# Kernel tuning notes

Measured on AMD Instinct MI355X. Metric: run time of the kernel, lower is better.

Reference implementation:

```python
import jax, jax.numpy as jnp
import numpy as np

NUM_HEADS = 12


def setup_inputs() -> dict:
    key = jax.random.key(0)
    ks = jax.random.split(key, 6)
    dim = 384
    B, N = 2048, 49
    nW = 64
    return {
        "x": jax.random.normal(ks[0], (B, N, dim), dtype=jnp.float32),
        "mask": jax.random.normal(ks[1], (nW, N, N), dtype=jnp.float32),
        "qkv_w": jax.random.normal(ks[2], (3 * dim, dim), dtype=jnp.float32) * 0.02,
        "qkv_b": jax.random.normal(ks[3], (3 * dim,), dtype=jnp.float32) * 0.02,
        "proj_w": jax.random.normal(ks[4], (dim, dim), dtype=jnp.float32) * 0.02,
        "proj_b": jax.random.normal(ks[5], (dim,), dtype=jnp.float32) * 0.02,
    }


def reference(x, mask, qkv_w, qkv_b, proj_w, proj_b):
    B, N, C = x.shape
    H = NUM_HEADS
    Dh = C // H
    scale = Dh ** -0.5
    nW = mask.shape[0]

    # qkv projection: [B, N, 3C]
    qkv = x @ qkv_w.T + qkv_b
    q, k, v = jnp.split(qkv, 3, axis=-1)

    def heads(t):  # [B, N, C] -> [B, H, N, Dh]
        return t.reshape(B, N, H, Dh).transpose(0, 2, 1, 3)

    q, k, v = heads(q) * scale, heads(k), heads(v)

    # [B, H, N, N] attention scores
    attn = jnp.einsum("bhnd,bhmd->bhnm", q, k)
    # add per-window additive mask: reshape B -> (B//nW, nW)
    attn = attn.reshape(B // nW, nW, H, N, N) + mask[None, :, None, :, :]
    attn = jax.nn.softmax(attn.reshape(B, H, N, N), axis=-1)

    out = jnp.einsum("bhnm,bhmd->bhnd", attn, v)
    out = out.transpose(0, 2, 1, 3).reshape(B, N, C)
    return out @ proj_w.T + proj_b
```

## Files before the change

### kernel.cpp

```cpp
#include <hip/hip_runtime.h>
#include <hip/hip_bf16.h>
#include <stdint.h>

typedef unsigned short u16;
typedef __attribute__((ext_vector_type(8))) short short8;
typedef __attribute__((ext_vector_type(4))) short s4v;
typedef __attribute__((ext_vector_type(4))) float f32x4;

__device__ inline u16 f2bf(float f) {
    union { float f; unsigned int u; } x; x.f = f;
    unsigned int u = x.u;
    unsigned int r = (u + 0x7FFFu + ((u >> 16) & 1u)) >> 16;
    return (u16)r;
}

__device__ inline void gld_lds16(const u16* g, u16* l) {
    auto const* gp = reinterpret_cast<const __attribute__((address_space(1))) unsigned int*>(
        reinterpret_cast<uintptr_t>(g));
    auto* lp = reinterpret_cast<__attribute__((address_space(3))) unsigned int*>(
        reinterpret_cast<uintptr_t>(l));
    __builtin_amdgcn_global_load_lds(gp, lp, 16, 0, 0);
}

#if __has_builtin(__builtin_amdgcn_mfma_f32_16x16x16bf16_1k)
#define MFMA16(a, b, c) __builtin_amdgcn_mfma_f32_16x16x16bf16_1k((a), (b), (c), 0, 0, 0)
#elif __has_builtin(__builtin_amdgcn_mfma_f32_16x16x16_bf16)
#define MFMA16(a, b, c) __builtin_amdgcn_mfma_f32_16x16x16_bf16((a), (b), (c), 0, 0, 0)
#else
__device__ inline f32x4 mfma16_asm(s4v a, s4v b, f32x4 c) {
    asm volatile("s_nop 1\n\tv_mfma_f32_16x16x16_bf16 %0, %1, %2, %0\n\ts_nop 7\n\ts_nop 7"
                 : "+v"(c) : "v"(a), "v"(b));
    return c;
}
#define MFMA16(a, b, c) mfma16_asm((a), (b), (c))
#endif

#define NX8 4816896
#define NQ8 55296
#define NP8 18432
__global__ __launch_bounds__(256) void prep_all(const float* __restrict__ x,
                                                const float* __restrict__ qw,
                                                const float* __restrict__ pw,
                                                u16* __restrict__ xb,
                                                u16* __restrict__ wq,
                                                u16* __restrict__ wp) {
    size_t i = (size_t)blockIdx.x * 256 + threadIdx.x;
    const float* src; u16* dst; size_t off;
    if (i < NX8)            { src = x;  dst = xb; off = i; }
    else if (i < NX8 + NQ8) { src = qw; dst = wq; off = i - NX8; }
    else                    { src = pw; dst = wp; off = i - (NX8 + NQ8); }
    float4 v0 = ((const float4*)src)[off * 2];
    float4 v1 = ((const float4*)src)[off * 2 + 1];
    u16 h[8];
    h[0] = f2bf(v0.x); h[1] = f2bf(v0.y); h[2] = f2bf(v0.z); h[3] = f2bf(v0.w);
    h[4] = f2bf(v1.x); h[5] = f2bf(v1.y); h[6] = f2bf(v1.z); h[7] = f2bf(v1.w);
    *(uint4*)(dst + off * 8) = *(const uint4*)h;
}

__global__ __launch_bounds__(256) void qkv_gemm(const u16* __restrict__ xb,
                                                const u16* __restrict__ wq,
                                                const float* __restrict__ bias,
                                                u16* __restrict__ qkv_out) {
    __shared__ u16 As[128 * 32];
    __shared__ u16 Bs[128 * 32];
    const int tid = threadIdx.x;
    const int wave = tid >> 6, lane = tid & 63;
    const int lr = lane >> 4, lc = lane & 15;
    const int wm = (wave & 1) * 64, wn = (wave >> 1) * 64;
    const int lin = blockIdx.x;
    const int xcd = lin & 7;
    const int idx = lin >> 3;
    const int nBase = (idx % 9) * 128;
    const int mBase = (xcd * 98 + idx / 9) * 128;

    f32x4 acc[4][4] = {};

    const int srow = lane >> 2, scol = (lane & 3) * 8;
    const u16* aSrc = xb + (size_t)(mBase + wave * 32 + srow) * 384 + scol;
    const u16* bSrc = wq + (size_t)(nBase + wave * 32 + srow) * 384 + scol;
    u16* aDst = &As[wave * 1024];
    u16* bDst = &Bs[wave * 1024];

    for (int k0 = 0; k0 < 384; k0 += 32) {
        gld_lds16(aSrc + k0, aDst);
        gld_lds16(aSrc + k0 + (size_t)16 * 384, aDst + 512);
        gld_lds16(bSrc + k0, bDst);
        gld_lds16(bSrc + k0 + (size_t)16 * 384, bDst + 512);
        __syncthreads();
        short8 af[4], bfr[4];
#pragma unroll
        for (int i = 0; i < 4; ++i)
            af[i] = *(const short8*)&As[(wm + i * 16 + lc) * 32 + lr * 8];
#pragma unroll
        for (int j = 0; j < 4; ++j)
            bfr[j] = *(const short8*)&Bs[(wn + j * 16 + lc) * 32 + lr * 8];
#pragma unroll
        for (int i = 0; i < 4; ++i)
#pragma unroll
            for (int j = 0; j < 4; ++j)
                acc[i][j] = __builtin_amdgcn_mfma_f32_16x16x32_bf16(bfr[j], af[i], acc[i][j], 0, 0, 0);
        __syncthreads();
    }

    const float scale = 0.17677669529663687f;
#pragma unroll
    for (int j = 0; j < 4; ++j) {
        int gnb = nBase + wn + j * 16 + lr * 4;
        float4 bv = *(const float4*)&bias[gnb];
        float mult = (gnb < 384) ? scale : 1.0f;
#pragma unroll
        for (int i = 0; i < 4; ++i) {
            int gm = mBase + wm + i * 16 + lc;
            union { u16 h[4]; uint2 u; } pk;
            pk.h[0] = f2bf((acc[i][j][0] + bv.x) * mult);
            pk.h[1] = f2bf((acc[i][j][1] + bv.y) * mult);
            pk.h[2] = f2bf((acc[i][j][2] + bv.z) * mult);
            pk.h[3] = f2bf((acc[i][j][3] + bv.w) * mult);
            *(uint2*)(qkv_out + (size_t)gm * 1152 + gnb) = pk.u;
        }
    }
}

__global__ __launch_bounds__(256, 3) void attn_kernel(const u16* __restrict__ qkv,
                                                      const float* __restrict__ mask,
                                                      u16* __restrict__ aout) {
#define PST 68
    __shared__ u16 Vt_s[4][32 * PST];
    const int tid = threadIdx.x;
    const int wave = tid >> 6, lane = tid & 63;
    const int lr = lane >> 4, lc = lane & 15;
    const int bid = blockIdx.x;
    const int b = bid / 3;
    const int h = (bid - b * 3) * 4 + wave;
    const int w = b & 63;
    const float* mrow = mask + (size_t)w * 2401;

    const u16* Q = qkv + (size_t)b * 49 * 1152 + h * 32;
    const u16* K = Q + 384;
    const u16* V = Q + 768;

    {
        u16 vv[32];
        if (lane < 49) {
#pragma unroll
            for (int c = 0; c < 4; ++c)
                *(uint4*)&vv[c * 8] = *(const uint4*)(V + (size_t)lane * 1152 + c * 8);
        } else {
#pragma unroll
            for (int c = 0; c < 32; ++c) vv[c] = 0;
        }
#pragma unroll
        for (int d = 0; d < 32; ++d)
            Vt_s[wave][d * PST + lane] = vv[d];
    }

    short8 qf[4], kf[4];
    const short8 z8 = {0, 0, 0, 0, 0, 0, 0, 0};
#pragma unroll
    for (int i = 0; i < 4; ++i) {
        int row = i * 16 + lc;
        qf[i] = (row < 49) ? *(const short8*)(Q + (size_t)row * 1152 + lr * 8) : z8;
        kf[i] = (row < 49) ? *(const short8*)(K + (size_t)row * 1152 + lr * 8) : z8;
    }

    __syncthreads();

    s4v vfA[2][4];
#pragma unroll
    for (int nt = 0; nt < 2; ++nt)
#pragma unroll
        for (int sj = 0; sj < 4; ++sj)
            vfA[nt][sj] = *(const s4v*)&Vt_s[wave][(nt * 16 + lc) * PST + sj * 16 + lr * 4];

    f32x4 S2[4][4] = {};
#pragma unroll
    for (int si = 0; si < 4; ++si)
#pragma unroll
        for (int sj = 0; sj < 4; ++sj)
            S2[si][sj] = __builtin_amdgcn_mfma_f32_16x16x32_bf16(kf[sj], qf[si], S2[si][sj], 0, 0, 0);

    const size_t orow = (size_t)b * 49 * 384 + h * 32 + lr * 4;
#pragma unroll
    for (int si = 0; si < 4; ++si) {
        int q = si * 16 + lc;
        int im = (q < 49) ? q : 48;
        const float* mq = mrow + im * 49;
        float s = 0.0f;
        s4v pfq[4];
#pragma unroll
        for (int sj = 0; sj < 4; ++sj) {
            int kbase = sj * 16 + lr * 4;
            s4v pk;
#pragma unroll
            for (int r = 0; r < 4; ++r) {
                int k = kbase + r;
                float t = (k < 49) ? (S2[si][sj][r] + mq[k]) : -1e30f;
                float p = __expf(t);
                s += p;
                pk[r] = (short)f2bf(p);
            }
            pfq[sj] = pk;
        }
        s += __shfl_xor(s, 16);
        s += __shfl_xor(s, 32);

        f32x4 O0 = {}, O1 = {};
#pragma unroll
        for (int sj = 0; sj < 4; ++sj) {
            O0 = MFMA16(vfA[0][sj], pfq[sj], O0);
            O1 = MFMA16(vfA[1][sj], pfq[sj], O1);
        }

        if (q < 49) {
            float rl = __builtin_amdgcn_rcpf(s);
            union { u16 h[4]; uint2 u; } pk;
            pk.h[0] = f2bf(O0[0] * rl); pk.h[1] = f2bf(O0[1] * rl);
            pk.h[2] = f2bf(O0[2] * rl); pk.h[3] = f2bf(O0[3] * rl);
            *(uint2*)(aout + orow + (size_t)q * 384) = pk.u;
            pk.h[0] = f2bf(O1[0] * rl); pk.h[1] = f2bf(O1[1] * rl);
            pk.h[2] = f2bf(O1[2] * rl); pk.h[3] = f2bf(O1[3] * rl);
            *(uint2*)(aout + orow + (size_t)q * 384 + 16) = pk.u;
        }
    }
#undef PST
}

__global__ __launch_bounds__(256) void proj_gemm(const u16* __restrict__ a,
                                                 const u16* __restrict__ wp,
                                                 const float* __restrict__ bias,
                                                 float* __restrict__ out) {
    __shared__ u16 As[128 * 32];
    __shared__ u16 Bs[128 * 32];
    const int tid = threadIdx.x;
    const int wave = tid >> 6, lane = tid & 63;
    const int lr = lane >> 4, lc = lane & 15;
    const int wm = (wave & 1) * 64, wn = (wave >> 1) * 64;
    const int lin = blockIdx.x;
    const int xcd = lin & 7;
    const int idx = lin >> 3;
    const int nBase = (idx % 3) * 128;
    const int mBase = (xcd * 98 + idx / 3) * 128;

    f32x4 acc[4][4] = {};

    const int srow = lane >> 2, scol = (lane & 3) * 8;
    const u16* aSrc = a  + (size_t)(mBase + wave * 32 + srow) * 384 + scol;
    const u16* bSrc = wp + (size_t)(nBase + wave * 32 + srow) * 384 + scol;
    u16* aDst = &As[wave * 1024];
    u16* bDst = &Bs[wave * 1024];

    for (int k0 = 0; k0 < 384; k0 += 32) {
        gld_lds16(aSrc + k0, aDst);
        gld_lds16(aSrc + k0 + (size_t)16 * 384, aDst + 512);
        gld_lds16(bSrc + k0, bDst);
        gld_lds16(bSrc + k0 + (size_t)16 * 384, bDst + 512);
        __syncthreads();
        short8 af[4], bfr[4];
#pragma unroll
        for (int i = 0; i < 4; ++i)
            af[i] = *(const short8*)&As[(wm + i * 16 + lc) * 32 + lr * 8];
#pragma unroll
        for (int j = 0; j < 4; ++j)
            bfr[j] = *(const short8*)&Bs[(wn + j * 16 + lc) * 32 + lr * 8];
#pragma unroll
        for (int i = 0; i < 4; ++i)
#pragma unroll
            for (int j = 0; j < 4; ++j)
                acc[i][j] = __builtin_amdgcn_mfma_f32_16x16x32_bf16(bfr[j], af[i], acc[i][j], 0, 0, 0);
        __syncthreads();
    }

#pragma unroll
    for (int j = 0; j < 4; ++j) {
        int gnb = nBase + wn + j * 16 + lr * 4;
        float4 bv = *(const float4*)&bias[gnb];
#pragma unroll
        for (int i = 0; i < 4; ++i) {
            int gm = mBase + wm + i * 16 + lc;
            float4 o;
            o.x = acc[i][j][0] + bv.x;
            o.y = acc[i][j][1] + bv.y;
            o.z = acc[i][j][2] + bv.z;
            o.w = acc[i][j][3] + bv.w;
            *(float4*)(out + (size_t)gm * 384 + gnb) = o;
        }
    }
}

extern "C" void kernel_launch(void* const* d_in, const int* in_sizes, int n_in,
                              void* d_out, int out_size, void* d_ws, size_t ws_size,
                              hipStream_t stream) {
    const float* x      = (const float*)d_in[0];
    const float* mask   = (const float*)d_in[1];
    const float* qkv_w  = (const float*)d_in[2];
    const float* qkv_b  = (const float*)d_in[3];
    const float* proj_w = (const float*)d_in[4];
    const float* proj_b = (const float*)d_in[5];
    float* out = (float*)d_out;

    char* ws = (char*)d_ws;
    u16* wq   = (u16*)ws;
    u16* wp   = (u16*)(ws + 884736);
    u16* qkvb = (u16*)(ws + 1179648);
    u16* xb   = (u16*)(ws + 232390656);
    u16* attn = xb;

    prep_all<<<19104, 256, 0, stream>>>(x, qkv_w, proj_w, xb, wq, wp);
    qkv_gemm<<<7056, 256, 0, stream>>>(xb, wq, qkv_b, qkvb);
    attn_kernel<<<6144, 256, 0, stream>>>(qkvb, mask, attn);
    proj_gemm<<<2352, 256, 0, stream>>>(attn, wp, proj_b, out);
}
```

Baseline: 570.1 us.

## Load GEMM operands directly into registers with prefetch instead of LDS staging

Both the QKV and projection GEMMs drop the shared-memory staging via global_load_lds and barriers. Each lane now loads its MFMA fragments straight from global memory and double-buffers the next k-slice in registers while the current MFMAs run. Launch bounds add a minimum of three blocks per CU. This removes LDS traffic and __syncthreads stalls, but waves now make redundant global loads of data shared across the block, which leans on L1/L2 and raises register pressure.

```diff
diff --git a/kernel.cpp b/kernel.cpp
--- a/kernel.cpp
+++ b/kernel.cpp
@@ -12,14 +12,6 @@
     unsigned int u = x.u;
     unsigned int r = (u + 0x7FFFu + ((u >> 16) & 1u)) >> 16;
     return (u16)r;
-}
-
-__device__ inline void gld_lds16(const u16* g, u16* l) {
-    auto const* gp = reinterpret_cast<const __attribute__((address_space(1))) unsigned int*>(
-        reinterpret_cast<uintptr_t>(g));
-    auto* lp = reinterpret_cast<__attribute__((address_space(3))) unsigned int*>(
-        reinterpret_cast<uintptr_t>(l));
-    __builtin_amdgcn_global_load_lds(gp, lp, 16, 0, 0);
 }
 
 #if __has_builtin(__builtin_amdgcn_mfma_f32_16x16x16bf16_1k)
@@ -57,12 +49,10 @@
     *(uint4*)(dst + off * 8) = *(const uint4*)h;
 }
 
-__global__ __launch_bounds__(256) void qkv_gemm(const u16* __restrict__ xb,
-                                                const u16* __restrict__ wq,
-                                                const float* __restrict__ bias,
-                                                u16* __restrict__ qkv_out) {
-    __shared__ u16 As[128 * 32];
-    __shared__ u16 Bs[128 * 32];
+__global__ __launch_bounds__(256, 3) void qkv_gemm(const u16* __restrict__ xb,
+                                                   const u16* __restrict__ wq,
+                                                   const float* __restrict__ bias,
+                                                   u16* __restrict__ qkv_out) {
     const int tid = threadIdx.x;
     const int wave = tid >> 6, lane = tid & 63;
     const int lr = lane >> 4, lc = lane & 15;
@@ -75,31 +65,34 @@
 
     f32x4 acc[4][4] = {};
 
-    const int srow = lane >> 2, scol = (lane & 3) * 8;
-    const u16* aSrc = xb + (size_t)(mBase + wave * 32 + srow) * 384 + scol;
-    const u16* bSrc = wq + (size_t)(nBase + wave * 32 + srow) * 384 + scol;
-    u16* aDst = &As[wave * 1024];
-    u16* bDst = &Bs[wave * 1024];
-
-    for (int k0 = 0; k0 < 384; k0 += 32) {
-        gld_lds16(aSrc + k0, aDst);
-        gld_lds16(aSrc + k0 + (size_t)16 * 384, aDst + 512);
-        gld_lds16(bSrc + k0, bDst);
-        gld_lds16(bSrc + k0 + (size_t)16 * 384, bDst + 512);
-        __syncthreads();
-        short8 af[4], bfr[4];
+    const u16* aP = xb + (size_t)(mBase + wm + lc) * 384 + lr * 8;
+    const u16* bP = wq + (size_t)(nBase + wn + lc) * 384 + lr * 8;
+
+    short8 aC[4], bC[4], aN[4], bN[4];
+#pragma unroll
+    for (int i = 0; i < 4; ++i) {
+        aC[i] = *(const short8*)(aP + (size_t)i * 16 * 384);
+        bC[i] = *(const short8*)(bP + (size_t)i * 16 * 384);
+    }
+#pragma unroll
+    for (int t = 0; t < 12; ++t) {
+        if (t < 11) {
+            const int k0 = (t + 1) * 32;
+#pragma unroll
+            for (int i = 0; i < 4; ++i) {
+                aN[i] = *(const short8*)(aP + (size_t)i * 16 * 384 + k0);
+                bN[i] = *(const short8*)(bP + (size_t)i * 16 * 384 + k0);
+            }
+        }
 #pragma unroll
         for (int i = 0; i < 4; ++i)
-            af[i] = *(const short8*)&As[(wm + i * 16 + lc) * 32 + lr * 8];
-#pragma unroll
-        for (int j = 0; j < 4; ++j)
-            bfr[j] = *(const short8*)&Bs[(wn + j * 16 + lc) * 32 + lr * 8];
-#pragma unroll
-        for (int i = 0; i < 4; ++i)
 #pragma unroll
             for (int j = 0; j < 4; ++j)
-                acc[i][j] = __builtin_amdgcn_mfma_f32_16x16x32_bf16(bfr[j], af[i], acc[i][j], 0, 0, 0);
-        __syncthreads();
+                acc[i][j] = __builtin_amdgcn_mfma_f32_16x16x32_bf16(bC[j], aC[i], acc[i][j], 0, 0, 0);
+        if (t < 11) {
+#pragma unroll
+            for (int i = 0; i < 4; ++i) { aC[i] = aN[i]; bC[i] = bN[i]; }
+        }
     }
 
     const float scale = 0.17677669529663687f;
@@ -225,12 +218,10 @@
 #undef PST
 }
 
-__global__ __launch_bounds__(256) void proj_gemm(const u16* __restrict__ a,
-                                                 const u16* __restrict__ wp,
-                                                 const float* __restrict__ bias,
-                                                 float* __restrict__ out) {
-    __shared__ u16 As[128 * 32];
-    __shared__ u16 Bs[128 * 32];
+__global__ __launch_bounds__(256, 3) void proj_gemm(const u16* __restrict__ a,
+                                                    const u16* __restrict__ wp,
+                                                    const float* __restrict__ bias,
+                                                    float* __restrict__ out) {
     const int tid = threadIdx.x;
     const int wave = tid >> 6, lane = tid & 63;
     const int lr = lane >> 4, lc = lane & 15;
@@ -243,31 +234,34 @@
 
     f32x4 acc[4][4] = {};
 
-    const int srow = lane >> 2, scol = (lane & 3) * 8;
-    const u16* aSrc = a  + (size_t)(mBase + wave * 32 + srow) * 384 + scol;
-    const u16* bSrc = wp + (size_t)(nBase + wave * 32 + srow) * 384 + scol;
-    u16* aDst = &As[wave * 1024];
-    u16* bDst = &Bs[wave * 1024];
-
-    for (int k0 = 0; k0 < 384; k0 += 32) {
-        gld_lds16(aSrc + k0, aDst);
-        gld_lds16(aSrc + k0 + (size_t)16 * 384, aDst + 512);
-        gld_lds16(bSrc + k0, bDst);
-        gld_lds16(bSrc + k0 + (size_t)16 * 384, bDst + 512);
-        __syncthreads();
-        short8 af[4], bfr[4];
+    const u16* aP = a  + (size_t)(mBase + wm + lc) * 384 + lr * 8;
+    const u16* bP = wp + (size_t)(nBase + wn + lc) * 384 + lr * 8;
+
+    short8 aC[4], bC[4], aN[4], bN[4];
+#pragma unroll
+    for (int i = 0; i < 4; ++i) {
+        aC[i] = *(const short8*)(aP + (size_t)i * 16 * 384);
+        bC[i] = *(const short8*)(bP + (size_t)i * 16 * 384);
+    }
+#pragma unroll
+    for (int t = 0; t < 12; ++t) {
+        if (t < 11) {
+            const int k0 = (t + 1) * 32;
+#pragma unroll
+            for (int i = 0; i < 4; ++i) {
+                aN[i] = *(const short8*)(aP + (size_t)i * 16 * 384 + k0);
+                bN[i] = *(const short8*)(bP + (size_t)i * 16 * 384 + k0);
+            }
+        }
 #pragma unroll
         for (int i = 0; i < 4; ++i)
-            af[i] = *(const short8*)&As[(wm + i * 16 + lc) * 32 + lr * 8];
-#pragma unroll
-        for (int j = 0; j < 4; ++j)
-            bfr[j] = *(const short8*)&Bs[(wn + j * 16 + lc) * 32 + lr * 8];
-#pragma unroll
-        for (int i = 0; i < 4; ++i)
 #pragma unroll
             for (int j = 0; j < 4; ++j)
-                acc[i][j] = __builtin_amdgcn_mfma_f32_16x16x32_bf16(bfr[j], af[i], acc[i][j], 0, 0, 0);
-        __syncthreads();
+                acc[i][j] = __builtin_amdgcn_mfma_f32_16x16x32_bf16(bC[j], aC[i], acc[i][j], 0, 0, 0);
+        if (t < 11) {
+#pragma unroll
+            for (int i = 0; i < 4; ++i) { aC[i] = aN[i]; bC[i] = bN[i]; }
+        }
     }
 
 #pragma unroll
```

New measurement: 797.3 us. +39.8%, slower.
